# Kernel optimization log

Hardware: AMD Instinct MI355X
Metric: run time of the kernel (lower is better)

Reference implementation:

```python
import jax, jax.numpy as jnp
import numpy as np
import math

DIM = 1024
MAX_SEQ_LEN = 8192

def setup_inputs() -> dict:
    key = jax.random.key(0)
    k1, k2, k3, k4 = jax.random.split(key, 4)
    x = jax.random.normal(k1, (4, 4096, DIM), dtype=jnp.float32)
    base_phases = jax.random.normal(k2, (MAX_SEQ_LEN, DIM), dtype=jnp.float32) * math.pi
    # nn.Linear(dim, dim): weight [out, in], bias [out]
    bound = 1.0 / math.sqrt(DIM)
    W = jax.random.uniform(k3, (DIM, DIM), dtype=jnp.float32, minval=-bound, maxval=bound)
    b = jax.random.uniform(k4, (DIM,), dtype=jnp.float32, minval=-bound, maxval=bound)
    return {"x": x, "base_phases": base_phases, "W": W, "b": b}

def reference(x, base_phases, W, b):
    B, L, D = x.shape
    phases = base_phases[:L][None, :, :]          # [1, L, D]
    value = jnp.einsum('bld,ed->ble', x, W) + b   # Linear: x @ W.T + b
    cos_p = jnp.cos(phases)
    sin_p = jnp.sin(phases)
    mem_real = jnp.cumsum(value * cos_p, axis=1)
    mem_imag = jnp.cumsum(value * sin_p, axis=1)
    retrieved = mem_real * cos_p + mem_imag * sin_p
    positions = jnp.arange(1, L + 1, dtype=jnp.float32)
    norm = jnp.sqrt(positions)[None, :, None]     # [1, L, 1]
    return retrieved / norm
```

## Files before the change

kernel.cpp:

```cpp
#include <hip/hip_runtime.h>
#include <hip/hip_bf16.h>

#define DIM 1024
#define SEQ 4096
#define NB 4
#define MROWS (NB * SEQ)
#define NC 64
#define CL (SEQ / NC)

#define BM 256
#define BN 256
#define BK 32
#define NTK 32
#define SLOTB 49152
#define GEMM_LDS (3 * SLOTB)
#define PHSTRIDE 1040

typedef __attribute__((ext_vector_type(8))) short bf16x8;
typedef __attribute__((ext_vector_type(4))) float f32x4;

static __device__ __forceinline__ unsigned short f2bf(float f) {
    union { float f; unsigned u; } v; v.f = f;
    unsigned r = v.u + 0x7FFF + ((v.u >> 16) & 1);
    return (unsigned short)(r >> 16);
}

static __device__ __forceinline__ float bf2f(unsigned short h) {
    union { unsigned u; float f; } v; v.u = ((unsigned)h) << 16;
    return v.f;
}

static __device__ __forceinline__ unsigned cvtpk(float a, float b) {
    unsigned r;
    asm("v_cvt_pk_bf16_f32 %0, %1, %2" : "=v"(r) : "v"(a), "v"(b));
    return r;
}

static __device__ __forceinline__ void gload_lds16(const void* g, void* l) {
    __builtin_amdgcn_global_load_lds((const __attribute__((address_space(1))) void*)g,
                                     (__attribute__((address_space(3))) void*)l, 16, 0, 0);
}

template<int CTRL>
static __device__ __forceinline__ float dppadd(float x) {
    int y = __builtin_amdgcn_update_dpp(0, __float_as_int(x), CTRL, 0xf, 0xf, true);
    return x + __int_as_float(y);
}
static __device__ __forceinline__ float rowreduce16(float x) {
    x = dppadd<0xB1>(x);
    x = dppadd<0x4E>(x);
    x = dppadd<0x141>(x);
    x = dppadd<0x140>(x);
    return x;
}

__global__ void convertW_kernel(const float* __restrict__ W, unsigned short* __restrict__ wb) {
    int t = blockIdx.x * 256 + threadIdx.x;
    float4 v = ((const float4*)W)[t];
    ushort4 o;
    o.x = f2bf(v.x); o.y = f2bf(v.y); o.z = f2bf(v.z); o.w = f2bf(v.w);
    ((ushort4*)wb)[t] = o;
}

static __device__ __forceinline__ void stage_Af32(const float* __restrict__ srcBase, char* smem,
                                                  int slot, int kt, int w, int lane) {
#pragma unroll
    for (int j = 0; j < 4; ++j) {
        const float* g = srcBase + (size_t)j * 8 * DIM + kt * BK;
        char* l = smem + (size_t)slot * SLOTB + (w * 4 + j) * 1024 + lane * 16;
        gload_lds16(g, l);
    }
}

static __device__ __forceinline__ void stage_B16(const unsigned short* __restrict__ srcBase, char* smem,
                                                 int slot, int kt, int w, int lane) {
#pragma unroll
    for (int r = 0; r < 2; ++r) {
        const unsigned short* g = srcBase + (size_t)r * 128 * DIM + kt * BK;
        char* l = smem + (size_t)slot * SLOTB + 32768 + (r * 128 + w * 16) * 64 + lane * 16;
        gload_lds16(g, l);
    }
}

__global__ __launch_bounds__(512, 2) void gemm_kernel(const float* __restrict__ X,
                                                      const unsigned short* __restrict__ Bm,
                                                      const float* __restrict__ bias,
                                                      const float* __restrict__ ph,
                                                      unsigned short* __restrict__ V,
                                                      float* __restrict__ pr,
                                                      float* __restrict__ pi) {
    extern __shared__ char smem[];
    const int tid  = threadIdx.x;
    const int lane = tid & 63;
    const int w    = tid >> 6;
    const int wm   = w >> 2;
    const int wr   = wm * 128;
    const int wc   = (w & 3) * 64;
    const int rl   = lane & 15;
    const int rh   = lane >> 4;
    const int m0   = blockIdx.x * BM;
    const int n0   = blockIdx.y * BN;

    const float* srcA = X + (size_t)(m0 + w * 32 + (lane >> 3)) * DIM + ((lane & 7) ^ (lane >> 3)) * 4;
    const unsigned short* srcB = Bm + (size_t)(n0 + w * 16 + (lane >> 2)) * DIM
                               + (((lane & 3) ^ ((lane >> 3) & 3)) * 8);

    const int swzB = (rh ^ ((rl >> 1) & 3)) * 16;
    const int aoff0 = (wr + rl) * 128 + (((rh * 2 + 0) ^ (rl & 7)) * 16);
    const int aoff1 = (wr + rl) * 128 + (((rh * 2 + 1) ^ (rl & 7)) * 16);

    f32x4 acc[8][4];
#pragma unroll
    for (int m = 0; m < 8; ++m)
#pragma unroll
        for (int n = 0; n < 4; ++n)
            acc[m][n] = (f32x4){0.f, 0.f, 0.f, 0.f};

    f32x4 bv4[4];
#pragma unroll
    for (int nf = 0; nf < 4; ++nf)
        bv4[nf] = *(const f32x4*)(bias + n0 + wc + nf * 16 + rh * 4);

    stage_Af32(srcA, smem, 0, 0, w, lane);
    stage_B16 (srcB, smem, 0, 0, w, lane);
    stage_Af32(srcA, smem, 1, 1, w, lane);
    stage_B16 (srcB, smem, 1, 1, w, lane);

#pragma unroll 1
    for (int t = 0; t < NTK; ++t) {
        asm volatile("s_waitcnt vmcnt(6)" ::: "memory");
        __builtin_amdgcn_s_barrier();
        const int sc = t % 3;
        const int ss = (t + 2) % 3;
        const int kn = (t + 2) & (NTK - 1);
        const char* sb = smem + (size_t)sc * SLOTB;

        bf16x8 bfr[4];
#pragma unroll
        for (int nf = 0; nf < 4; ++nf)
            bfr[nf] = *(const bf16x8*)(sb + 32768 + (wc + nf * 16 + rl) * 64 + swzB);

        bf16x8 af[4];
#pragma unroll
        for (int mf = 0; mf < 4; ++mf) {
            f32x4 q0 = *(const f32x4*)(sb + mf * 2048 + aoff0);
            f32x4 q1 = *(const f32x4*)(sb + mf * 2048 + aoff1);
            union { unsigned u[4]; bf16x8 v; } cv;
            cv.u[0] = cvtpk(q0[0], q0[1]); cv.u[1] = cvtpk(q0[2], q0[3]);
            cv.u[2] = cvtpk(q1[0], q1[1]); cv.u[3] = cvtpk(q1[2], q1[3]);
            af[mf] = cv.v;
        }
        stage_Af32(srcA, smem, ss, kn, w, lane);
        __builtin_amdgcn_s_setprio(1);
#pragma unroll
        for (int mf = 0; mf < 4; ++mf)
#pragma unroll
            for (int nf = 0; nf < 4; ++nf)
                acc[mf][nf] = __builtin_amdgcn_mfma_f32_16x16x32_bf16(bfr[nf], af[mf], acc[mf][nf], 0, 0, 0);
        __builtin_amdgcn_s_setprio(0);

#pragma unroll
        for (int mf = 0; mf < 4; ++mf) {
            f32x4 q0 = *(const f32x4*)(sb + (mf + 4) * 2048 + aoff0);
            f32x4 q1 = *(const f32x4*)(sb + (mf + 4) * 2048 + aoff1);
            union { unsigned u[4]; bf16x8 v; } cv;
            cv.u[0] = cvtpk(q0[0], q0[1]); cv.u[1] = cvtpk(q0[2], q0[3]);
            cv.u[2] = cvtpk(q1[0], q1[1]); cv.u[3] = cvtpk(q1[2], q1[3]);
            af[mf] = cv.v;
        }
        stage_B16(srcB, smem, ss, kn, w, lane);
        __builtin_amdgcn_s_setprio(1);
#pragma unroll
        for (int mf = 0; mf < 4; ++mf)
#pragma unroll
            for (int nf = 0; nf < 4; ++nf)
                acc[mf + 4][nf] = __builtin_amdgcn_mfma_f32_16x16x32_bf16(bfr[nf], af[mf], acc[mf + 4][nf], 0, 0, 0);
        __builtin_amdgcn_s_setprio(0);
    }

    asm volatile("s_waitcnt vmcnt(0)" ::: "memory");
    __builtin_amdgcn_s_barrier();

#pragma unroll
    for (int mf = 0; mf < 8; ++mf)
#pragma unroll
        for (int nf = 0; nf < 4; ++nf)
#pragma unroll
            for (int j = 0; j < 4; ++j)
                acc[mf][nf][j] += bv4[nf][j];

    const int bb    = m0 >> 12;
    const int lbase = m0 & (SEQ - 1);
    const int lb    = lbase + wr;
    float csr[2][4][4], csi[2][4][4];
#pragma unroll
    for (int h = 0; h < 2; ++h)
#pragma unroll
        for (int nf = 0; nf < 4; ++nf)
#pragma unroll
            for (int j = 0; j < 4; ++j) { csr[h][nf][j] = 0.f; csi[h][nf][j] = 0.f; }

#pragma unroll
    for (int h = 0; h < 2; ++h) {
#pragma unroll
        for (int q = 0; q < 16; ++q) {
            const int idx = q * 512 + tid;
            const int row = idx >> 6;
            const int cl  = idx & 63;
            const int grow = lbase + ((row >> 6) << 7) + h * 64 + (row & 63);
            gload_lds16(ph + (size_t)grow * DIM + n0 + cl * 4,
                        smem + row * PHSTRIDE + cl * 16);
        }
#pragma unroll
        for (int mf4 = 0; mf4 < 4; ++mf4) {
            const int mf   = h * 4 + mf4;
            const int grow = m0 + wr + mf * 16 + rl;
#pragma unroll
            for (int nf = 0; nf < 4; ++nf) {
                const int gcol0 = n0 + wc + nf * 16 + rh * 4;
                ushort4 o;
                o.x = f2bf(acc[mf][nf][0]); o.y = f2bf(acc[mf][nf][1]);
                o.z = f2bf(acc[mf][nf][2]); o.w = f2bf(acc[mf][nf][3]);
                *(ushort4*)(V + (size_t)grow * DIM + gcol0) = o;
            }
        }
        asm volatile("s_waitcnt vmcnt(0)" ::: "memory");
        __builtin_amdgcn_s_barrier();
#pragma unroll
        for (int mf4 = 0; mf4 < 4; ++mf4) {
            const int mf     = h * 4 + mf4;
            const int ldsrow = wm * 64 + mf4 * 16 + rl;
#pragma unroll
            for (int nf = 0; nf < 4; ++nf) {
                const int cch = (wc >> 2) + nf * 4 + rh;
                f32x4 pp = *(const f32x4*)(smem + ldsrow * PHSTRIDE + cch * 16);
#pragma unroll
                for (int j = 0; j < 4; ++j) {
                    float s, cn;
                    __sincosf(pp[j], &s, &cn);
                    csr[h][nf][j] += acc[mf][nf][j] * cn;
                    csi[h][nf][j] += acc[mf][nf][j] * s;
                }
            }
        }
        __builtin_amdgcn_s_barrier();
    }

#pragma unroll
    for (int h = 0; h < 2; ++h)
#pragma unroll
        for (int nf = 0; nf < 4; ++nf)
#pragma unroll
            for (int j = 0; j < 4; ++j) {
                csr[h][nf][j] = rowreduce16(csr[h][nf][j]);
                csi[h][nf][j] = rowreduce16(csi[h][nf][j]);
            }
    if (rl == 0) {
#pragma unroll
        for (int h = 0; h < 2; ++h) {
            const int c = (lb + h * 64) >> 6;
            const size_t base = ((size_t)bb * NC + c) * DIM;
#pragma unroll
            for (int nf = 0; nf < 4; ++nf) {
                const int gcol0 = n0 + wc + nf * 16 + rh * 4;
                *(float4*)(pr + base + gcol0) =
                    (float4){csr[h][nf][0], csr[h][nf][1], csr[h][nf][2], csr[h][nf][3]};
                *(float4*)(pi + base + gcol0) =
                    (float4){csi[h][nf][0], csi[h][nf][1], csi[h][nf][2], csi[h][nf][3]};
            }
        }
    }
}

__global__ void passB_kernel(float* __restrict__ pr, float* __restrict__ pi) {
    int t = blockIdx.x * 256 + threadIdx.x;
    int bb = t >> 10;
    int e  = t & 1023;
    float r = 0.f, im = 0.f;
    for (int c = 0; c < NC; ++c) {
        size_t idx = ((size_t)bb * NC + c) * DIM + e;
        float tr = pr[idx], ti = pi[idx];
        pr[idx] = r; pi[idx] = im;
        r += tr; im += ti;
    }
}

__global__ void passC_kernel(const unsigned short* __restrict__ val, const float* __restrict__ ph,
                             const float* __restrict__ pr, const float* __restrict__ pi,
                             float* __restrict__ out) {
    int t  = blockIdx.x * 256 + threadIdx.x;
    int c  = blockIdx.y;
    int bb = blockIdx.z;
    size_t base = ((size_t)bb * SEQ + (size_t)c * CL) * (DIM / 2) + t;
    const ushort2* v = (const ushort2*)val + base;
    const float2*  p = (const float2*)ph + (size_t)c * CL * (DIM / 2) + t;
    float2* o = (float2*)out + base;
    size_t pidx = ((size_t)bb * NC + c) * DIM + 2 * t;
    float ar0 = pr[pidx], ar1 = pr[pidx + 1];
    float ai0 = pi[pidx], ai1 = pi[pidx + 1];
    const int l0 = c * CL;
    for (int l = 0; l < CL; ++l) {
        ushort2 vv = v[(size_t)l * (DIM / 2)];
        float2  pp = p[(size_t)l * (DIM / 2)];
        float v0 = bf2f(vv.x), v1 = bf2f(vv.y);
        float s0, c0, s1, c1;
        __sincosf(pp.x, &s0, &c0);
        __sincosf(pp.y, &s1, &c1);
        ar0 += v0 * c0; ai0 += v0 * s0;
        ar1 += v1 * c1; ai1 += v1 * s1;
        float rn = rsqrtf((float)(l0 + l + 1));
        float2 ov;
        ov.x = (ar0 * c0 + ai0 * s0) * rn;
        ov.y = (ar1 * c1 + ai1 * s1) * rn;
        o[(size_t)l * (DIM / 2)] = ov;
    }
}

extern "C" void kernel_launch(void* const* d_in, const int* in_sizes, int n_in,
                              void* d_out, int out_size, void* d_ws, size_t ws_size,
                              hipStream_t stream) {
    const float* x  = (const float*)d_in[0];
    const float* ph = (const float*)d_in[1];
    const float* W  = (const float*)d_in[2];
    const float* b  = (const float*)d_in[3];
    float* out = (float*)d_out;

    unsigned short* vb = (unsigned short*)d_ws;
    unsigned short* wb = vb + (size_t)MROWS * DIM;
    float* pr = (float*)(wb + (size_t)DIM * DIM);
    float* pi = pr + (size_t)NB * NC * DIM;

    (void)hipFuncSetAttribute((const void*)gemm_kernel,
                              hipFuncAttributeMaxDynamicSharedMemorySize, GEMM_LDS);

    convertW_kernel<<<DIM * DIM / 4 / 256, 256, 0, stream>>>(W, wb);
    {
        dim3 grid(MROWS / BM, DIM / BN);
        gemm_kernel<<<grid, 512, GEMM_LDS, stream>>>(x, wb, b, ph, vb, pr, pi);
    }
    passB_kernel<<<16, 256, 0, stream>>>(pr, pi);
    {
        dim3 grid(DIM / 512, NC, NB);
        passC_kernel<<<grid, 256, 0, stream>>>(vb, ph, pr, pi, out);
    }
}
```

Measured before the change: 85.33 us.

## Fuse GEMM, chunk-prefix scan and output pass into one persistent kernel

Merges the GEMM, the chunk carry scan and the per-row output pass into a single kernel joined by two software grid barriers. The GEMM accumulators stay in registers, so the bf16 value tensor is no longer written and read back. Within-chunk cumulative sums use DPP lane scans, and the carry scan over 64 chunks becomes a wave-level scan. The change relies on all 256 blocks being co-resident for the spin barrier and now reads phases straight from global memory instead of staging them through LDS.

```diff
diff --git a/kernel.cpp b/kernel.cpp
--- a/kernel.cpp
+++ b/kernel.cpp
@@ -14,7 +14,7 @@
 #define NTK 32
 #define SLOTB 49152
 #define GEMM_LDS (3 * SLOTB)
-#define PHSTRIDE 1040
+#define NBLK 256
 
 typedef __attribute__((ext_vector_type(8))) short bf16x8;
 typedef __attribute__((ext_vector_type(4))) float f32x4;
@@ -25,11 +25,6 @@
     return (unsigned short)(r >> 16);
 }
 
-static __device__ __forceinline__ float bf2f(unsigned short h) {
-    union { unsigned u; float f; } v; v.u = ((unsigned)h) << 16;
-    return v.f;
-}
-
 static __device__ __forceinline__ unsigned cvtpk(float a, float b) {
     unsigned r;
     asm("v_cvt_pk_bf16_f32 %0, %1, %2" : "=v"(r) : "v"(a), "v"(b));
@@ -41,17 +36,52 @@
                                      (__attribute__((address_space(3))) void*)l, 16, 0, 0);
 }
 
-template<int CTRL>
-static __device__ __forceinline__ float dppadd(float x) {
-    int y = __builtin_amdgcn_update_dpp(0, __float_as_int(x), CTRL, 0xf, 0xf, true);
-    return x + __int_as_float(y);
+template<int CTRL, int ROWM>
+static __device__ __forceinline__ float dppterm(float x) {
+    int y = __builtin_amdgcn_update_dpp(0, __float_as_int(x), CTRL, ROWM, 0xf, true);
+    return __int_as_float(y);
 }
 static __device__ __forceinline__ float rowreduce16(float x) {
-    x = dppadd<0xB1>(x);
-    x = dppadd<0x4E>(x);
-    x = dppadd<0x141>(x);
-    x = dppadd<0x140>(x);
+    x += dppterm<0xB1, 0xf>(x);
+    x += dppterm<0x4E, 0xf>(x);
+    x += dppterm<0x141, 0xf>(x);
+    x += dppterm<0x140, 0xf>(x);
     return x;
+}
+static __device__ __forceinline__ float scan16(float x) {
+    x += dppterm<0x111, 0xf>(x);
+    x += dppterm<0x112, 0xf>(x);
+    x += dppterm<0x114, 0xf>(x);
+    x += dppterm<0x118, 0xf>(x);
+    return x;
+}
+static __device__ __forceinline__ float scan64(float x) {
+    x += dppterm<0x111, 0xf>(x);
+    x += dppterm<0x112, 0xf>(x);
+    x += dppterm<0x114, 0xf>(x);
+    x += dppterm<0x118, 0xf>(x);
+    x += dppterm<0x142, 0xa>(x);
+    x += dppterm<0x143, 0xc>(x);
+    return x;
+}
+
+static __device__ __forceinline__ void grid_sync(int* gbar) {
+    __syncthreads();
+    __threadfence();
+    if (threadIdx.x == 0) {
+        int gen = __hip_atomic_load(gbar + 2, __ATOMIC_ACQUIRE, __HIP_MEMORY_SCOPE_AGENT);
+        int idx = gen & 1;
+        int arrived = __hip_atomic_fetch_add(gbar + idx, 1, __ATOMIC_ACQ_REL, __HIP_MEMORY_SCOPE_AGENT) + 1;
+        if (arrived == NBLK) {
+            __hip_atomic_store(gbar + idx, 0, __ATOMIC_RELAXED, __HIP_MEMORY_SCOPE_AGENT);
+            __hip_atomic_store(gbar + 2, gen + 1, __ATOMIC_RELEASE, __HIP_MEMORY_SCOPE_AGENT);
+        } else {
+            while (__hip_atomic_load(gbar + 2, __ATOMIC_ACQUIRE, __HIP_MEMORY_SCOPE_AGENT) == gen)
+                __builtin_amdgcn_s_sleep(1);
+        }
+    }
+    __syncthreads();
+    __threadfence();
 }
 
 __global__ void convertW_kernel(const float* __restrict__ W, unsigned short* __restrict__ wb) {
@@ -82,13 +112,14 @@
     }
 }
 
-__global__ __launch_bounds__(512, 2) void gemm_kernel(const float* __restrict__ X,
+__global__ __launch_bounds__(512, 2) void mega_kernel(const float* __restrict__ X,
                                                       const unsigned short* __restrict__ Bm,
                                                       const float* __restrict__ bias,
                                                       const float* __restrict__ ph,
-                                                      unsigned short* __restrict__ V,
                                                       float* __restrict__ pr,
-                                                      float* __restrict__ pi) {
+                                                      float* __restrict__ pi,
+                                                      float* __restrict__ out,
+                                                      int* __restrict__ gbar) {
     extern __shared__ char smem[];
     const int tid  = threadIdx.x;
     const int lane = tid & 63;
@@ -178,9 +209,6 @@
         __builtin_amdgcn_s_setprio(0);
     }
 
-    asm volatile("s_waitcnt vmcnt(0)" ::: "memory");
-    __builtin_amdgcn_s_barrier();
-
 #pragma unroll
     for (int mf = 0; mf < 8; ++mf)
 #pragma unroll
@@ -192,127 +220,126 @@
     const int bb    = m0 >> 12;
     const int lbase = m0 & (SEQ - 1);
     const int lb    = lbase + wr;
-    float csr[2][4][4], csi[2][4][4];
-#pragma unroll
-    for (int h = 0; h < 2; ++h)
-#pragma unroll
-        for (int nf = 0; nf < 4; ++nf)
-#pragma unroll
-            for (int j = 0; j < 4; ++j) { csr[h][nf][j] = 0.f; csi[h][nf][j] = 0.f; }
-
-#pragma unroll
-    for (int h = 0; h < 2; ++h) {
-#pragma unroll
-        for (int q = 0; q < 16; ++q) {
-            const int idx = q * 512 + tid;
-            const int row = idx >> 6;
-            const int cl  = idx & 63;
-            const int grow = lbase + ((row >> 6) << 7) + h * 64 + (row & 63);
-            gload_lds16(ph + (size_t)grow * DIM + n0 + cl * 4,
-                        smem + row * PHSTRIDE + cl * 16);
-        }
-#pragma unroll
-        for (int mf4 = 0; mf4 < 4; ++mf4) {
-            const int mf   = h * 4 + mf4;
-            const int grow = m0 + wr + mf * 16 + rl;
+
+    {
+        float csr[2][4][4], csi[2][4][4];
+#pragma unroll
+        for (int h = 0; h < 2; ++h)
+#pragma unroll
+            for (int nf = 0; nf < 4; ++nf)
+#pragma unroll
+                for (int j = 0; j < 4; ++j) { csr[h][nf][j] = 0.f; csi[h][nf][j] = 0.f; }
+#pragma unroll
+        for (int mf = 0; mf < 8; ++mf) {
+            const int l = lb + mf * 16 + rl;
+            const int half = mf >> 2;
 #pragma unroll
             for (int nf = 0; nf < 4; ++nf) {
                 const int gcol0 = n0 + wc + nf * 16 + rh * 4;
-                ushort4 o;
-                o.x = f2bf(acc[mf][nf][0]); o.y = f2bf(acc[mf][nf][1]);
-                o.z = f2bf(acc[mf][nf][2]); o.w = f2bf(acc[mf][nf][3]);
-                *(ushort4*)(V + (size_t)grow * DIM + gcol0) = o;
-            }
-        }
-        asm volatile("s_waitcnt vmcnt(0)" ::: "memory");
-        __builtin_amdgcn_s_barrier();
-#pragma unroll
-        for (int mf4 = 0; mf4 < 4; ++mf4) {
-            const int mf     = h * 4 + mf4;
-            const int ldsrow = wm * 64 + mf4 * 16 + rl;
-#pragma unroll
-            for (int nf = 0; nf < 4; ++nf) {
-                const int cch = (wc >> 2) + nf * 4 + rh;
-                f32x4 pp = *(const f32x4*)(smem + ldsrow * PHSTRIDE + cch * 16);
+                f32x4 pp = *(const f32x4*)(ph + (size_t)l * DIM + gcol0);
 #pragma unroll
                 for (int j = 0; j < 4; ++j) {
                     float s, cn;
                     __sincosf(pp[j], &s, &cn);
-                    csr[h][nf][j] += acc[mf][nf][j] * cn;
-                    csi[h][nf][j] += acc[mf][nf][j] * s;
+                    csr[half][nf][j] += acc[mf][nf][j] * cn;
+                    csi[half][nf][j] += acc[mf][nf][j] * s;
                 }
             }
         }
-        __builtin_amdgcn_s_barrier();
-    }
-
+#pragma unroll
+        for (int h = 0; h < 2; ++h)
+#pragma unroll
+            for (int nf = 0; nf < 4; ++nf)
+#pragma unroll
+                for (int j = 0; j < 4; ++j) {
+                    csr[h][nf][j] = rowreduce16(csr[h][nf][j]);
+                    csi[h][nf][j] = rowreduce16(csi[h][nf][j]);
+                }
+        if (rl == 0) {
+#pragma unroll
+            for (int h = 0; h < 2; ++h) {
+                const int c = (lb >> 6) + h;
+                const size_t base = ((size_t)bb * NC + c) * DIM;
+#pragma unroll
+                for (int nf = 0; nf < 4; ++nf) {
+                    const int gcol0 = n0 + wc + nf * 16 + rh * 4;
+                    *(float4*)(pr + base + gcol0) =
+                        (float4){csr[h][nf][0], csr[h][nf][1], csr[h][nf][2], csr[h][nf][3]};
+                    *(float4*)(pi + base + gcol0) =
+                        (float4){csi[h][nf][0], csi[h][nf][1], csi[h][nf][2], csi[h][nf][3]};
+                }
+            }
+        }
+    }
+
+    grid_sync(gbar);
+
+    {
+        const int bid = blockIdx.y * 64 + blockIdx.x;
+        const int wid = bid * 8 + w;
+#pragma unroll
+        for (int s = 0; s < 2; ++s) {
+            const int task = wid * 2 + s;
+            const int b = task >> 10;
+            const int e = task & 1023;
+            const size_t idx = (size_t)(b * NC + lane) * DIM + e;
+            float r  = pr[idx];
+            float im = pi[idx];
+            pr[idx] = scan64(r) - r;
+            pi[idx] = scan64(im) - im;
+        }
+    }
+
+    grid_sync(gbar);
+
+    float rns[2][4];
 #pragma unroll
     for (int h = 0; h < 2; ++h)
 #pragma unroll
-        for (int nf = 0; nf < 4; ++nf)
+        for (int q = 0; q < 4; ++q)
+            rns[h][q] = rsqrtf((float)(lb + h * 64 + q * 16 + rl + 1));
+
+#pragma unroll
+    for (int h = 0; h < 2; ++h) {
+        const int c = (lb >> 6) + h;
+        const size_t pbase = ((size_t)bb * NC + c) * DIM;
+#pragma unroll
+        for (int nf = 0; nf < 4; ++nf) {
+            const int gcol0 = n0 + wc + nf * 16 + rh * 4;
+            f32x4 preR = *(const f32x4*)(pr + pbase + gcol0);
+            f32x4 preI = *(const f32x4*)(pi + pbase + gcol0);
+            float sn[4][4], cs[4][4];
+#pragma unroll
+            for (int q = 0; q < 4; ++q) {
+                const int l = lb + h * 64 + q * 16 + rl;
+                f32x4 pp = *(const f32x4*)(ph + (size_t)l * DIM + gcol0);
+#pragma unroll
+                for (int j = 0; j < 4; ++j)
+                    __sincosf(pp[j], &sn[q][j], &cs[q][j]);
+            }
+            float ov[4][4];
 #pragma unroll
             for (int j = 0; j < 4; ++j) {
-                csr[h][nf][j] = rowreduce16(csr[h][nf][j]);
-                csi[h][nf][j] = rowreduce16(csi[h][nf][j]);
-            }
-    if (rl == 0) {
-#pragma unroll
-        for (int h = 0; h < 2; ++h) {
-            const int c = (lb + h * 64) >> 6;
-            const size_t base = ((size_t)bb * NC + c) * DIM;
-#pragma unroll
-            for (int nf = 0; nf < 4; ++nf) {
-                const int gcol0 = n0 + wc + nf * 16 + rh * 4;
-                *(float4*)(pr + base + gcol0) =
-                    (float4){csr[h][nf][0], csr[h][nf][1], csr[h][nf][2], csr[h][nf][3]};
-                *(float4*)(pi + base + gcol0) =
-                    (float4){csi[h][nf][0], csi[h][nf][1], csi[h][nf][2], csi[h][nf][3]};
-            }
-        }
-    }
-}
-
-__global__ void passB_kernel(float* __restrict__ pr, float* __restrict__ pi) {
-    int t = blockIdx.x * 256 + threadIdx.x;
-    int bb = t >> 10;
-    int e  = t & 1023;
-    float r = 0.f, im = 0.f;
-    for (int c = 0; c < NC; ++c) {
-        size_t idx = ((size_t)bb * NC + c) * DIM + e;
-        float tr = pr[idx], ti = pi[idx];
-        pr[idx] = r; pi[idx] = im;
-        r += tr; im += ti;
-    }
-}
-
-__global__ void passC_kernel(const unsigned short* __restrict__ val, const float* __restrict__ ph,
-                             const float* __restrict__ pr, const float* __restrict__ pi,
-                             float* __restrict__ out) {
-    int t  = blockIdx.x * 256 + threadIdx.x;
-    int c  = blockIdx.y;
-    int bb = blockIdx.z;
-    size_t base = ((size_t)bb * SEQ + (size_t)c * CL) * (DIM / 2) + t;
-    const ushort2* v = (const ushort2*)val + base;
-    const float2*  p = (const float2*)ph + (size_t)c * CL * (DIM / 2) + t;
-    float2* o = (float2*)out + base;
-    size_t pidx = ((size_t)bb * NC + c) * DIM + 2 * t;
-    float ar0 = pr[pidx], ar1 = pr[pidx + 1];
-    float ai0 = pi[pidx], ai1 = pi[pidx + 1];
-    const int l0 = c * CL;
-    for (int l = 0; l < CL; ++l) {
-        ushort2 vv = v[(size_t)l * (DIM / 2)];
-        float2  pp = p[(size_t)l * (DIM / 2)];
-        float v0 = bf2f(vv.x), v1 = bf2f(vv.y);
-        float s0, c0, s1, c1;
-        __sincosf(pp.x, &s0, &c0);
-        __sincosf(pp.y, &s1, &c1);
-        ar0 += v0 * c0; ai0 += v0 * s0;
-        ar1 += v1 * c1; ai1 += v1 * s1;
-        float rn = rsqrtf((float)(l0 + l + 1));
-        float2 ov;
-        ov.x = (ar0 * c0 + ai0 * s0) * rn;
-        ov.y = (ar1 * c1 + ai1 * s1) * rn;
-        o[(size_t)l * (DIM / 2)] = ov;
+                float cR = preR[j];
+                float cI = preI[j];
+#pragma unroll
+                for (int q = 0; q < 4; ++q) {
+                    float v  = acc[h * 4 + q][nf][j];
+                    float vR = v * cs[q][j];
+                    float vI = v * sn[q][j];
+                    float cumR = scan16(vR) + cR;
+                    float cumI = scan16(vI) + cI;
+                    ov[q][j] = (cumR * cs[q][j] + cumI * sn[q][j]) * rns[h][q];
+                    if (q < 3) { cR += rowreduce16(vR); cI += rowreduce16(vI); }
+                }
+            }
+#pragma unroll
+            for (int q = 0; q < 4; ++q) {
+                const int l = lb + h * 64 + q * 16 + rl;
+                *(float4*)(out + ((size_t)bb * SEQ + l) * DIM + gcol0) =
+                    (float4){ov[q][0], ov[q][1], ov[q][2], ov[q][3]};
+            }
+        }
     }
 }
 
@@ -325,22 +352,18 @@
     const float* b  = (const float*)d_in[3];
     float* out = (float*)d_out;
 
-    unsigned short* vb = (unsigned short*)d_ws;
-    unsigned short* wb = vb + (size_t)MROWS * DIM;
+    unsigned short* wb = (unsigned short*)d_ws;
     float* pr = (float*)(wb + (size_t)DIM * DIM);
     float* pi = pr + (size_t)NB * NC * DIM;
-
-    (void)hipFuncSetAttribute((const void*)gemm_kernel,
+    int* gbar = (int*)(pi + (size_t)NB * NC * DIM);
+
+    (void)hipFuncSetAttribute((const void*)mega_kernel,
                               hipFuncAttributeMaxDynamicSharedMemorySize, GEMM_LDS);
 
+    hipMemsetAsync(gbar, 0, 3 * sizeof(int), stream);
     convertW_kernel<<<DIM * DIM / 4 / 256, 256, 0, stream>>>(W, wb);
     {
         dim3 grid(MROWS / BM, DIM / BN);
-        gemm_kernel<<<grid, 512, GEMM_LDS, stream>>>(x, wb, b, ph, vb, pr, pi);
-    }
-    passB_kernel<<<16, 256, 0, stream>>>(pr, pi);
-    {
-        dim3 grid(DIM / 512, NC, NB);
-        passC_kernel<<<grid, 256, 0, stream>>>(vb, ph, pr, pi, out);
-    }
-}
+        mega_kernel<<<grid, 512, GEMM_LDS, stream>>>(x, wb, b, ph, pr, pi, out, gbar);
+    }
+}
```

Result: slower. 294.5 us (+245.1%).
